# Kernel optimization log

Measured on AMD Instinct MI355X. Metric: run time of the kernel, lower is better.

Reference implementation:

```python
import jax, jax.numpy as jnp
import numpy as np

B, S, H, D = 32, 127, 4, 64
HD = H * D
SCALE = 1.0 / np.sqrt(D).astype(np.float32)
NEG = -100000.0


def _remove_mask_keep(seq_len):
    # For q>=3, rows are grouped in 2-row blocks starting at i=3,5,...;
    # each block may only attend (among k>=3) to its own two columns.
    q = jnp.arange(seq_len)[:, None]
    k = jnp.arange(seq_len)[None, :]
    blk = 3 + 2 * ((q - 3) // 2)
    return (q < 3) | (k < 3) | ((k >= blk) & (k < blk + 2))  # [S, S] bool


def setup_inputs() -> dict:
    rng = jax.random.key(0)
    ks = jax.random.split(rng, 16)
    n = lambda k, shape: jax.random.normal(k, shape, dtype=jnp.float32)
    w = 1.0 / np.sqrt(HD).astype(np.float32)
    return {
        "query": n(ks[0], (B, S, HD)),
        "key": n(ks[1], (B, S, HD)),
        "value": n(ks[2], (B, S, HD)),
        "graph": jax.random.randint(ks[3], (B, S, S), 0, 2, dtype=jnp.int32),
        "edge_key": n(ks[4], (B, S, S, D)),
        "edge_value": n(ks[5], (B, S, S, D)),
        "edge_query": n(ks[6], (B, S, S, D)),
        "Wq": n(ks[7], (HD, HD)) * w, "bq": jnp.zeros((HD,), jnp.float32),
        "Wk": n(ks[8], (HD, HD)) * w, "bk": jnp.zeros((HD,), jnp.float32),
        "Wv": n(ks[9], (HD, HD)) * w, "bv": jnp.zeros((HD,), jnp.float32),
        "Wo": n(ks[10], (HD, HD)) * w, "bo": jnp.zeros((HD,), jnp.float32),
    }


def reference(query, key, value, graph, edge_key, edge_value, edge_query,
              Wq, bq, Wk, bk, Wv, bv, Wo, bo):
    b, s, _ = query.shape
    q = (query @ Wq.T + bq).reshape(b, s, H, D)
    k = (key @ Wk.T + bk).reshape(b, s, H, D)
    v = (value @ Wv.T + bv).reshape(b, s, H, D)

    scores = (
        jnp.einsum('bqhd,bkhd->bhqk', q, k)
        + jnp.einsum('bqhd,bqkd->bhqk', q, edge_key)
        + jnp.einsum('bkqd,bkhd->bhqk', edge_query, k)
        + jnp.einsum('bkqd,bqkd->bqk', edge_query, edge_key)[:, None]
    ) * SCALE

    mask = (graph != 0)[:, None, :, :] & _remove_mask_keep(s)[None, None]
    scores = jnp.where(mask, scores, NEG)
    attn = jax.nn.softmax(scores, axis=-1)  # dropout p=0 -> identity

    x = (jnp.einsum('bhqk,bkhd->bqhd', attn, v)
         + jnp.einsum('bhqk,bqkd->bqhd', attn, edge_value)).reshape(b, s, HD)
    return x @ Wo.T + bo
```

## Files before the change

### kernel.cpp

```cpp
#include <hip/hip_runtime.h>
#include <hip/hip_bf16.h>

#define S_LEN 127
#define NB    32
#define HDIM  256
#define DH    64
#define SCALE_F 0.125f

typedef __bf16 bf16x8 __attribute__((ext_vector_type(8)));
typedef __bf16 bf16x4 __attribute__((ext_vector_type(4)));
typedef float  f32x4  __attribute__((ext_vector_type(4)));

#define NTOK  4064
#define NQKV4 260096
#define NW4   16384

__global__ __launch_bounds__(256) void convert_bf16(
    const float* __restrict__ q, const float* __restrict__ k,
    const float* __restrict__ v,
    const float* __restrict__ Wq, const float* __restrict__ Wk,
    const float* __restrict__ Wv, const float* __restrict__ Wo,
    __bf16* __restrict__ qb, __bf16* __restrict__ kb, __bf16* __restrict__ vb,
    __bf16* __restrict__ Wqb, __bf16* __restrict__ Wkb,
    __bf16* __restrict__ Wvb, __bf16* __restrict__ Wob)
{
  size_t t = (size_t)blockIdx.x * 256 + threadIdx.x;
  const float* src; __bf16* dst;
  if (t < NQKV4)               { src = q;  dst = qb;  }
  else if ((t -= NQKV4) < NQKV4) { src = k;  dst = kb;  }
  else if ((t -= NQKV4) < NQKV4) { src = v;  dst = vb;  }
  else if ((t -= NQKV4) < NW4)   { src = Wq; dst = Wqb; }
  else if ((t -= NW4) < NW4)     { src = Wk; dst = Wkb; }
  else if ((t -= NW4) < NW4)     { src = Wv; dst = Wvb; }
  else if ((t -= NW4) < NW4)     { src = Wo; dst = Wob; }
  else return;
  const float4 x = ((const float4*)src)[t];
  bf16x4 r;
  r[0] = (__bf16)x.x; r[1] = (__bf16)x.y; r[2] = (__bf16)x.z; r[3] = (__bf16)x.w;
  ((bf16x4*)dst)[t] = r;
}

__device__ __forceinline__ void gemm_tile32_bf16(
    const __bf16* __restrict__ A, const __bf16* __restrict__ W,
    const float* __restrict__ bias, float* __restrict__ out,
    int row0, int col0)
{
  const int lane = threadIdx.x & 63;
  const int r  = lane & 15;
  const int ks = (lane >> 4) << 3;
  const __bf16* Ab = A + (size_t)(row0 + r) * HDIM + ks;
  const __bf16* Wb = W + (size_t)(col0 + r) * HDIM + ks;
  f32x4 acc[2][2] = {};

  bf16x8 ca[2], cw[2];
  ca[0] = *(const bf16x8*)Ab;
  ca[1] = *(const bf16x8*)(Ab + (size_t)16 * HDIM);
  cw[0] = *(const bf16x8*)Wb;
  cw[1] = *(const bf16x8*)(Wb + (size_t)16 * HDIM);
#pragma unroll
  for (int kb = 0; kb < 8; ++kb) {
    bf16x8 na[2], nw[2];
    if (kb < 7) {
      const int off = (kb + 1) * 32;
      na[0] = *(const bf16x8*)(Ab + off);
      na[1] = *(const bf16x8*)(Ab + (size_t)16 * HDIM + off);
      nw[0] = *(const bf16x8*)(Wb + off);
      nw[1] = *(const bf16x8*)(Wb + (size_t)16 * HDIM + off);
    }
#pragma unroll
    for (int mi = 0; mi < 2; ++mi)
#pragma unroll
      for (int ni = 0; ni < 2; ++ni)
        acc[mi][ni] = __builtin_amdgcn_mfma_f32_16x16x32_bf16(
            ca[mi], cw[ni], acc[mi][ni], 0, 0, 0);
    if (kb < 7) {
      ca[0] = na[0]; ca[1] = na[1];
      cw[0] = nw[0]; cw[1] = nw[1];
    }
  }
  const int crow = (lane >> 4) * 4;
  const int ccol = lane & 15;
#pragma unroll
  for (int mi = 0; mi < 2; ++mi)
#pragma unroll
    for (int ni = 0; ni < 2; ++ni) {
      const int oc = col0 + ni * 16 + ccol;
      const float bv = bias[oc];
#pragma unroll
      for (int rg = 0; rg < 4; ++rg)
        out[(size_t)(row0 + mi * 16 + crow + rg) * HDIM + oc] = acc[mi][ni][rg] + bv;
    }
}

__global__ __launch_bounds__(256) void gemm_qkv(
    const __bf16* __restrict__ qb, const __bf16* __restrict__ kb,
    const __bf16* __restrict__ vb,
    const __bf16* __restrict__ Wqb, const float* __restrict__ bq,
    const __bf16* __restrict__ Wkb, const float* __restrict__ bk,
    const __bf16* __restrict__ Wvb, const float* __restrict__ bv,
    float* __restrict__ qp, float* __restrict__ kp, float* __restrict__ vp)
{
  const int w = threadIdx.x >> 6;
  const int tile = blockIdx.x * 4 + w;
  if (tile >= 127) return;
  const __bf16* A; const __bf16* W; const float* bias; float* o;
  if (blockIdx.z == 0)      { A = qb; W = Wqb; bias = bq; o = qp; }
  else if (blockIdx.z == 1) { A = kb; W = Wkb; bias = bk; o = kp; }
  else                      { A = vb; W = Wvb; bias = bv; o = vp; }
  gemm_tile32_bf16(A, W, bias, o, tile * 32, blockIdx.y * 32);
}

__global__ __launch_bounds__(256) void gemm_o(
    const __bf16* __restrict__ A, const __bf16* __restrict__ W,
    const float* __restrict__ bias, float* __restrict__ out)
{
  const int w = threadIdx.x >> 6;
  const int tile = blockIdx.x * 4 + w;
  if (tile >= 127) return;
  gemm_tile32_bf16(A, W, bias, out, tile * 32, blockIdx.y * 32);
}

__global__ __launch_bounds__(256) void attn_kernel(
    const float* __restrict__ qp, const float* __restrict__ kp,
    const float* __restrict__ vp, const int* __restrict__ graph,
    const float* __restrict__ ekt, const float* __restrict__ evt,
    const float* __restrict__ eqt, __bf16* __restrict__ xpb)
{
  int b, q;
  {
    const int bx = blockIdx.x;
    if (bx < 96) { b = bx / 3; q = bx % 3; }
    else { const int rr = bx - 96; b = rr / 124; q = 3 + rr % 124; }
  }
  const int t = threadIdx.x;
  const int w = t >> 6;
  const int l = t & 63;
  const int ll = l & 15;
  const int g  = l >> 4;

  __shared__ int   s_list[S_LEN];
  __shared__ float s_attn[4][S_LEN];
  __shared__ int   s_cnt[2];

  bool valid = false;
  const int k0 = w * 64 + l;
  if (w < 2 && k0 < S_LEN) {
    const int gr = graph[((size_t)b * S_LEN + q) * S_LEN + k0];
    bool keep;
    if (q < 3 || k0 < 3) keep = true;
    else {
      const int blk = 3 + 2 * ((q - 3) >> 1);
      keep = (k0 >= blk) & (k0 < blk + 2);
    }
    valid = (gr != 0) && keep;
  }
  const unsigned long long bal = __ballot(valid);
  if (w < 2 && l == 0) s_cnt[w] = (int)__popcll(bal);
  __syncthreads();
  int n = s_cnt[0] + s_cnt[1];
  if (valid) {
    const int pos = (int)__popcll(bal & ((1ull << l) - 1ull)) + (w ? s_cnt[0] : 0);
    s_list[pos] = k0;
  }
  __syncthreads();

  if (n == 0) {
    if (t < S_LEN) {
      s_list[t] = t;
      const float u = 1.0f / 127.0f;
      s_attn[0][t] = u; s_attn[1][t] = u; s_attn[2][t] = u; s_attn[3][t] = u;
    }
    n = S_LEN;
  } else {
    const float* qrow = qp + ((size_t)b * S_LEN + q) * HDIM;
    float4 q4[4];
#pragma unroll
    for (int h = 0; h < 4; ++h)
      q4[h] = *(const float4*)(qrow + h * 64 + ll * 4);
    const float* eqb = eqt + ((size_t)b * S_LEN * S_LEN + q) * DH;
    const float* ekb = ekt + ((size_t)(b * S_LEN + q)) * S_LEN * DH;
    const float* kpb = kp + (size_t)b * S_LEN * HDIM;

    for (int i0 = 0; i0 < n; i0 += 16) {
      const int i = i0 + w * 4 + g;
      float p0 = 0.f, p1 = 0.f, p2 = 0.f, p3 = 0.f;
      if (i < n) {
        const int kk = s_list[i];
        const float4 eq4 = *(const float4*)(eqb + (size_t)kk * (S_LEN * DH) + ll * 4);
        const float4 ek4 = *(const float4*)(ekb + kk * DH + ll * 4);
        const float* kr = kpb + (size_t)kk * HDIM + ll * 4;
        const float4 kh0 = *(const float4*)(kr);
        const float4 kh1 = *(const float4*)(kr + 64);
        const float4 kh2 = *(const float4*)(kr + 128);
        const float4 kh3 = *(const float4*)(kr + 192);
        const float tx = ek4.x, ty = ek4.y, tz = ek4.z, tw = ek4.w;
        const float s0x = q4[0].x + eq4.x, s0y = q4[0].y + eq4.y,
                    s0z = q4[0].z + eq4.z, s0w = q4[0].w + eq4.w;
        const float s1x = q4[1].x + eq4.x, s1y = q4[1].y + eq4.y,
                    s1z = q4[1].z + eq4.z, s1w = q4[1].w + eq4.w;
        const float s2x = q4[2].x + eq4.x, s2y = q4[2].y + eq4.y,
                    s2z = q4[2].z + eq4.z, s2w = q4[2].w + eq4.w;
        const float s3x = q4[3].x + eq4.x, s3y = q4[3].y + eq4.y,
                    s3z = q4[3].z + eq4.z, s3w = q4[3].w + eq4.w;
        p0 = s0x*(kh0.x+tx) + s0y*(kh0.y+ty) + s0z*(kh0.z+tz) + s0w*(kh0.w+tw);
        p1 = s1x*(kh1.x+tx) + s1y*(kh1.y+ty) + s1z*(kh1.z+tz) + s1w*(kh1.w+tw);
        p2 = s2x*(kh2.x+tx) + s2y*(kh2.y+ty) + s2z*(kh2.z+tz) + s2w*(kh2.w+tw);
        p3 = s3x*(kh3.x+tx) + s3y*(kh3.y+ty) + s3z*(kh3.z+tz) + s3w*(kh3.w+tw);
      }
#pragma unroll
      for (int off = 1; off < 16; off <<= 1) {
        p0 += __shfl_xor(p0, off, 64);
        p1 += __shfl_xor(p1, off, 64);
        p2 += __shfl_xor(p2, off, 64);
        p3 += __shfl_xor(p3, off, 64);
      }
      if (i < n && ll < 4) {
        const float s = (ll == 0) ? p0 : (ll == 1) ? p1 : (ll == 2) ? p2 : p3;
        s_attn[ll][i] = s * SCALE_F;
      }
    }
    __syncthreads();

    {
      const float v0 = (l < n) ? s_attn[w][l] : -INFINITY;
      const float v1 = (64 + l < n) ? s_attn[w][64 + l] : -INFINITY;
      float mx = fmaxf(v0, v1);
#pragma unroll
      for (int off = 32; off; off >>= 1) mx = fmaxf(mx, __shfl_xor(mx, off, 64));
      const float e0 = (l < n) ? expf(v0 - mx) : 0.f;
      const float e1 = (64 + l < n) ? expf(v1 - mx) : 0.f;
      float sm = e0 + e1;
#pragma unroll
      for (int off = 32; off; off >>= 1) sm += __shfl_xor(sm, off, 64);
      const float inv = 1.0f / sm;
      if (l < n) s_attn[w][l] = e0 * inv;
      if (64 + l < n) s_attn[w][64 + l] = e1 * inv;
    }
  }
  __syncthreads();

  {
    const float* evb = evt + ((size_t)(b * S_LEN + q)) * S_LEN * DH;
    const float* vbp = vp + (size_t)b * S_LEN * HDIM + w * DH + ll * 4;
    float ax = 0.f, ay = 0.f, az = 0.f, aw = 0.f;
    for (int i0 = 0; i0 < n; i0 += 4) {
      const int i = i0 + g;
      if (i < n) {
        const int kk = s_list[i];
        const float a = s_attn[w][i];
        const float4 v4 = *(const float4*)(vbp + (size_t)kk * HDIM);
        const float4 e4 = *(const float4*)(evb + kk * DH + ll * 4);
        ax += a * (v4.x + e4.x);
        ay += a * (v4.y + e4.y);
        az += a * (v4.z + e4.z);
        aw += a * (v4.w + e4.w);
      }
    }
#pragma unroll
    for (int off = 16; off < 64; off <<= 1) {
      ax += __shfl_xor(ax, off, 64);
      ay += __shfl_xor(ay, off, 64);
      az += __shfl_xor(az, off, 64);
      aw += __shfl_xor(aw, off, 64);
    }
    if (g == 0) {
      bf16x4 r;
      r[0] = (__bf16)ax; r[1] = (__bf16)ay; r[2] = (__bf16)az; r[3] = (__bf16)aw;
      *(bf16x4*)(xpb + ((size_t)b * S_LEN + q) * HDIM + w * 64 + ll * 4) = r;
    }
  }
}

extern "C" void kernel_launch(void* const* d_in, const int* in_sizes, int n_in,
                              void* d_out, int out_size, void* d_ws, size_t ws_size,
                              hipStream_t stream) {
  const float* query = (const float*)d_in[0];
  const float* key   = (const float*)d_in[1];
  const float* value = (const float*)d_in[2];
  const int*   graph = (const int*)d_in[3];
  const float* ekt   = (const float*)d_in[4];
  const float* evt   = (const float*)d_in[5];
  const float* eqt   = (const float*)d_in[6];
  const float* Wq = (const float*)d_in[7];  const float* bq = (const float*)d_in[8];
  const float* Wk = (const float*)d_in[9];  const float* bk = (const float*)d_in[10];
  const float* Wv = (const float*)d_in[11]; const float* bv = (const float*)d_in[12];
  const float* Wo = (const float*)d_in[13]; const float* bo = (const float*)d_in[14];
  float* out = (float*)d_out;

  const size_t NE = (size_t)NTOK * HDIM;
  char* p = (char*)d_ws;
  float* qp = (float*)p;            p += NE * 4;
  float* kp = (float*)p;            p += NE * 4;
  float* vp = (float*)p;            p += NE * 4;
  __bf16* qb  = (__bf16*)p;         p += NE * 2;
  __bf16* kb  = (__bf16*)p;         p += NE * 2;
  __bf16* vb  = (__bf16*)p;         p += NE * 2;
  __bf16* xpb = (__bf16*)p;         p += NE * 2;
  __bf16* Wqb = (__bf16*)p;         p += (size_t)HDIM * HDIM * 2;
  __bf16* Wkb = (__bf16*)p;         p += (size_t)HDIM * HDIM * 2;
  __bf16* Wvb = (__bf16*)p;         p += (size_t)HDIM * HDIM * 2;
  __bf16* Wob = (__bf16*)p;

  convert_bf16<<<dim3(3304), 256, 0, stream>>>(query, key, value,
                                               Wq, Wk, Wv, Wo,
                                               qb, kb, vb, Wqb, Wkb, Wvb, Wob);
  gemm_qkv<<<dim3(32, 8, 3), 256, 0, stream>>>(qb, kb, vb,
                                               Wqb, bq, Wkb, bk, Wvb, bv,
                                               qp, kp, vp);
  attn_kernel<<<dim3(NB * S_LEN), 256, 0, stream>>>(qp, kp, vp, graph,
                                                    ekt, evt, eqt, xpb);
  gemm_o<<<dim3(32, 8), 256, 0, stream>>>(xpb, Wob, bo, out);
}
```

Before: 52.76 us.

## Fuse activation bf16 conversion into QKV GEMM, store projections as bf16, prefetch attention loads

The QKV GEMM now reads the fp32 activations directly and converts them to bf16 into shared memory, so the separate activation-conversion pass and its bf16 copies are gone. Each block computes a 32x256 output tile with one wave per 64 columns. Q/K/V projections are stored as bf16 instead of fp32, which halves their write and gather traffic in the attention kernel. The attention score and value loops now software-prefetch the next iteration's gathered loads, at the cost of more registers and extra rounding of the projections.

```diff
diff --git a/kernel.cpp b/kernel.cpp
--- a/kernel.cpp
+++ b/kernel.cpp
@@ -12,39 +12,113 @@
 typedef float  f32x4  __attribute__((ext_vector_type(4)));
 
 #define NTOK  4064
-#define NQKV4 260096
 #define NW4   16384
 
-__global__ __launch_bounds__(256) void convert_bf16(
-    const float* __restrict__ q, const float* __restrict__ k,
-    const float* __restrict__ v,
+__device__ __forceinline__ float4 b2f4(bf16x4 v) {
+  return make_float4((float)v[0], (float)v[1], (float)v[2], (float)v[3]);
+}
+
+__global__ __launch_bounds__(256) void convert_w(
     const float* __restrict__ Wq, const float* __restrict__ Wk,
     const float* __restrict__ Wv, const float* __restrict__ Wo,
-    __bf16* __restrict__ qb, __bf16* __restrict__ kb, __bf16* __restrict__ vb,
     __bf16* __restrict__ Wqb, __bf16* __restrict__ Wkb,
     __bf16* __restrict__ Wvb, __bf16* __restrict__ Wob)
 {
   size_t t = (size_t)blockIdx.x * 256 + threadIdx.x;
   const float* src; __bf16* dst;
-  if (t < NQKV4)               { src = q;  dst = qb;  }
-  else if ((t -= NQKV4) < NQKV4) { src = k;  dst = kb;  }
-  else if ((t -= NQKV4) < NQKV4) { src = v;  dst = vb;  }
-  else if ((t -= NQKV4) < NW4)   { src = Wq; dst = Wqb; }
-  else if ((t -= NW4) < NW4)     { src = Wk; dst = Wkb; }
-  else if ((t -= NW4) < NW4)     { src = Wv; dst = Wvb; }
-  else if ((t -= NW4) < NW4)     { src = Wo; dst = Wob; }
-  else return;
+  if (t < NW4)                 { src = Wq; dst = Wqb; }
+  else if ((t -= NW4) < NW4)   { src = Wk; dst = Wkb; }
+  else if ((t -= NW4) < NW4)   { src = Wv; dst = Wvb; }
+  else { t -= NW4;               src = Wo; dst = Wob; }
   const float4 x = ((const float4*)src)[t];
   bf16x4 r;
   r[0] = (__bf16)x.x; r[1] = (__bf16)x.y; r[2] = (__bf16)x.z; r[3] = (__bf16)x.w;
   ((bf16x4*)dst)[t] = r;
 }
 
-__device__ __forceinline__ void gemm_tile32_bf16(
+__global__ __launch_bounds__(256) void gemm_qkv(
+    const float* __restrict__ q_in, const float* __restrict__ k_in,
+    const float* __restrict__ v_in,
+    const __bf16* __restrict__ Wqb, const float* __restrict__ bq,
+    const __bf16* __restrict__ Wkb, const float* __restrict__ bk,
+    const __bf16* __restrict__ Wvb, const float* __restrict__ bv,
+    __bf16* __restrict__ qpb, __bf16* __restrict__ kpb, __bf16* __restrict__ vpb)
+{
+  const int tile = blockIdx.x;
+  const float* A; const __bf16* W; const float* bias; __bf16* o;
+  if (blockIdx.y == 0)      { A = q_in; W = Wqb; bias = bq; o = qpb; }
+  else if (blockIdx.y == 1) { A = k_in; W = Wkb; bias = bk; o = kpb; }
+  else                      { A = v_in; W = Wvb; bias = bv; o = vpb; }
+
+  __shared__ __bf16 sA[32][264];
+  const int row0 = tile * 32;
+
+#pragma unroll
+  for (int j = 0; j < 8; ++j) {
+    const int f = threadIdx.x + j * 256;
+    const int rr = f >> 6, c4 = f & 63;
+    const float4 x = *(const float4*)(A + (size_t)(row0 + rr) * HDIM + c4 * 4);
+    __bf16* d = &sA[rr][c4 * 4];
+    d[0] = (__bf16)x.x; d[1] = (__bf16)x.y; d[2] = (__bf16)x.z; d[3] = (__bf16)x.w;
+  }
+  __syncthreads();
+
+  const int w    = threadIdx.x >> 6;
+  const int lane = threadIdx.x & 63;
+  const int r    = lane & 15;
+  const int ksl  = (lane >> 4) << 3;
+  const int wc   = w * 64;
+
+  const __bf16* Wb = W + (size_t)(wc + r) * HDIM + ksl;
+  f32x4 acc[2][4] = {};
+
+  bf16x8 cw[4];
+#pragma unroll
+  for (int ni = 0; ni < 4; ++ni)
+    cw[ni] = *(const bf16x8*)(Wb + (size_t)ni * 16 * HDIM);
+#pragma unroll
+  for (int kb = 0; kb < 8; ++kb) {
+    bf16x8 nw[4];
+    if (kb < 7) {
+#pragma unroll
+      for (int ni = 0; ni < 4; ++ni)
+        nw[ni] = *(const bf16x8*)(Wb + (size_t)ni * 16 * HDIM + (kb + 1) * 32);
+    }
+    const bf16x8 a0 = *(const bf16x8*)&sA[r][kb * 32 + ksl];
+    const bf16x8 a1 = *(const bf16x8*)&sA[16 + r][kb * 32 + ksl];
+#pragma unroll
+    for (int ni = 0; ni < 4; ++ni) {
+      acc[0][ni] = __builtin_amdgcn_mfma_f32_16x16x32_bf16(a0, cw[ni], acc[0][ni], 0, 0, 0);
+      acc[1][ni] = __builtin_amdgcn_mfma_f32_16x16x32_bf16(a1, cw[ni], acc[1][ni], 0, 0, 0);
+    }
+    if (kb < 7) {
+#pragma unroll
+      for (int ni = 0; ni < 4; ++ni) cw[ni] = nw[ni];
+    }
+  }
+  const int crow = (lane >> 4) * 4;
+  const int ccol = lane & 15;
+#pragma unroll
+  for (int mi = 0; mi < 2; ++mi)
+#pragma unroll
+    for (int ni = 0; ni < 4; ++ni) {
+      const int oc = wc + ni * 16 + ccol;
+      const float bv = bias[oc];
+#pragma unroll
+      for (int rg = 0; rg < 4; ++rg)
+        o[(size_t)(row0 + mi * 16 + crow + rg) * HDIM + oc] =
+            (__bf16)(acc[mi][ni][rg] + bv);
+    }
+}
+
+__global__ __launch_bounds__(256) void gemm_o(
     const __bf16* __restrict__ A, const __bf16* __restrict__ W,
-    const float* __restrict__ bias, float* __restrict__ out,
-    int row0, int col0)
+    const float* __restrict__ bias, float* __restrict__ out)
 {
+  const int w = threadIdx.x >> 6;
+  const int tile = blockIdx.x * 4 + w;
+  if (tile >= 127) return;
+  const int row0 = tile * 32, col0 = blockIdx.y * 32;
   const int lane = threadIdx.x & 63;
   const int r  = lane & 15;
   const int ks = (lane >> 4) << 3;
@@ -92,37 +166,9 @@
     }
 }
 
-__global__ __launch_bounds__(256) void gemm_qkv(
-    const __bf16* __restrict__ qb, const __bf16* __restrict__ kb,
-    const __bf16* __restrict__ vb,
-    const __bf16* __restrict__ Wqb, const float* __restrict__ bq,
-    const __bf16* __restrict__ Wkb, const float* __restrict__ bk,
-    const __bf16* __restrict__ Wvb, const float* __restrict__ bv,
-    float* __restrict__ qp, float* __restrict__ kp, float* __restrict__ vp)
-{
-  const int w = threadIdx.x >> 6;
-  const int tile = blockIdx.x * 4 + w;
-  if (tile >= 127) return;
-  const __bf16* A; const __bf16* W; const float* bias; float* o;
-  if (blockIdx.z == 0)      { A = qb; W = Wqb; bias = bq; o = qp; }
-  else if (blockIdx.z == 1) { A = kb; W = Wkb; bias = bk; o = kp; }
-  else                      { A = vb; W = Wvb; bias = bv; o = vp; }
-  gemm_tile32_bf16(A, W, bias, o, tile * 32, blockIdx.y * 32);
-}
-
-__global__ __launch_bounds__(256) void gemm_o(
-    const __bf16* __restrict__ A, const __bf16* __restrict__ W,
-    const float* __restrict__ bias, float* __restrict__ out)
-{
-  const int w = threadIdx.x >> 6;
-  const int tile = blockIdx.x * 4 + w;
-  if (tile >= 127) return;
-  gemm_tile32_bf16(A, W, bias, out, tile * 32, blockIdx.y * 32);
-}
-
 __global__ __launch_bounds__(256) void attn_kernel(
-    const float* __restrict__ qp, const float* __restrict__ kp,
-    const float* __restrict__ vp, const int* __restrict__ graph,
+    const __bf16* __restrict__ qpb, const __bf16* __restrict__ kpb,
+    const __bf16* __restrict__ vpb, const int* __restrict__ graph,
     const float* __restrict__ ekt, const float* __restrict__ evt,
     const float* __restrict__ eqt, __bf16* __restrict__ xpb)
 {
@@ -172,40 +218,55 @@
     }
     n = S_LEN;
   } else {
-    const float* qrow = qp + ((size_t)b * S_LEN + q) * HDIM;
+    const __bf16* qrow = qpb + ((size_t)b * S_LEN + q) * HDIM;
     float4 q4[4];
 #pragma unroll
     for (int h = 0; h < 4; ++h)
-      q4[h] = *(const float4*)(qrow + h * 64 + ll * 4);
-    const float* eqb = eqt + ((size_t)b * S_LEN * S_LEN + q) * DH;
-    const float* ekb = ekt + ((size_t)(b * S_LEN + q)) * S_LEN * DH;
-    const float* kpb = kp + (size_t)b * S_LEN * HDIM;
-
+      q4[h] = b2f4(*(const bf16x4*)(qrow + h * 64 + ll * 4));
+    const float* eqb2 = eqt + ((size_t)b * S_LEN * S_LEN + q) * DH;
+    const float* ekb2 = ekt + ((size_t)(b * S_LEN + q)) * S_LEN * DH;
+    const __bf16* kpbb = kpb + (size_t)b * S_LEN * HDIM;
+    const int myi = w * 4 + g;
+
+    float4 ceq, cek;
+    bf16x4 ck0, ck1, ck2, ck3;
+    if (myi < n) {
+      const int kk = s_list[myi];
+      ceq = *(const float4*)(eqb2 + (size_t)kk * (S_LEN * DH) + ll * 4);
+      cek = *(const float4*)(ekb2 + kk * DH + ll * 4);
+      const __bf16* kr = kpbb + (size_t)kk * HDIM + ll * 4;
+      ck0 = *(const bf16x4*)(kr);
+      ck1 = *(const bf16x4*)(kr + 64);
+      ck2 = *(const bf16x4*)(kr + 128);
+      ck3 = *(const bf16x4*)(kr + 192);
+    }
     for (int i0 = 0; i0 < n; i0 += 16) {
-      const int i = i0 + w * 4 + g;
+      const int i = i0 + myi;
+      float4 neq, nek;
+      bf16x4 nk0, nk1, nk2, nk3;
+      const int j = i + 16;
+      if (j < n) {
+        const int kk = s_list[j];
+        neq = *(const float4*)(eqb2 + (size_t)kk * (S_LEN * DH) + ll * 4);
+        nek = *(const float4*)(ekb2 + kk * DH + ll * 4);
+        const __bf16* kr = kpbb + (size_t)kk * HDIM + ll * 4;
+        nk0 = *(const bf16x4*)(kr);
+        nk1 = *(const bf16x4*)(kr + 64);
+        nk2 = *(const bf16x4*)(kr + 128);
+        nk3 = *(const bf16x4*)(kr + 192);
+      }
       float p0 = 0.f, p1 = 0.f, p2 = 0.f, p3 = 0.f;
       if (i < n) {
-        const int kk = s_list[i];
-        const float4 eq4 = *(const float4*)(eqb + (size_t)kk * (S_LEN * DH) + ll * 4);
-        const float4 ek4 = *(const float4*)(ekb + kk * DH + ll * 4);
-        const float* kr = kpb + (size_t)kk * HDIM + ll * 4;
-        const float4 kh0 = *(const float4*)(kr);
-        const float4 kh1 = *(const float4*)(kr + 64);
-        const float4 kh2 = *(const float4*)(kr + 128);
-        const float4 kh3 = *(const float4*)(kr + 192);
-        const float tx = ek4.x, ty = ek4.y, tz = ek4.z, tw = ek4.w;
-        const float s0x = q4[0].x + eq4.x, s0y = q4[0].y + eq4.y,
-                    s0z = q4[0].z + eq4.z, s0w = q4[0].w + eq4.w;
-        const float s1x = q4[1].x + eq4.x, s1y = q4[1].y + eq4.y,
-                    s1z = q4[1].z + eq4.z, s1w = q4[1].w + eq4.w;
-        const float s2x = q4[2].x + eq4.x, s2y = q4[2].y + eq4.y,
-                    s2z = q4[2].z + eq4.z, s2w = q4[2].w + eq4.w;
-        const float s3x = q4[3].x + eq4.x, s3y = q4[3].y + eq4.y,
-                    s3z = q4[3].z + eq4.z, s3w = q4[3].w + eq4.w;
-        p0 = s0x*(kh0.x+tx) + s0y*(kh0.y+ty) + s0z*(kh0.z+tz) + s0w*(kh0.w+tw);
-        p1 = s1x*(kh1.x+tx) + s1y*(kh1.y+ty) + s1z*(kh1.z+tz) + s1w*(kh1.w+tw);
-        p2 = s2x*(kh2.x+tx) + s2y*(kh2.y+ty) + s2z*(kh2.z+tz) + s2w*(kh2.w+tw);
-        p3 = s3x*(kh3.x+tx) + s3y*(kh3.y+ty) + s3z*(kh3.z+tz) + s3w*(kh3.w+tw);
+        const float4 k0f = b2f4(ck0), k1f = b2f4(ck1),
+                     k2f = b2f4(ck2), k3f = b2f4(ck3);
+        p0 = (q4[0].x+ceq.x)*(k0f.x+cek.x) + (q4[0].y+ceq.y)*(k0f.y+cek.y)
+           + (q4[0].z+ceq.z)*(k0f.z+cek.z) + (q4[0].w+ceq.w)*(k0f.w+cek.w);
+        p1 = (q4[1].x+ceq.x)*(k1f.x+cek.x) + (q4[1].y+ceq.y)*(k1f.y+cek.y)
+           + (q4[1].z+ceq.z)*(k1f.z+cek.z) + (q4[1].w+ceq.w)*(k1f.w+cek.w);
+        p2 = (q4[2].x+ceq.x)*(k2f.x+cek.x) + (q4[2].y+ceq.y)*(k2f.y+cek.y)
+           + (q4[2].z+ceq.z)*(k2f.z+cek.z) + (q4[2].w+ceq.w)*(k2f.w+cek.w);
+        p3 = (q4[3].x+ceq.x)*(k3f.x+cek.x) + (q4[3].y+ceq.y)*(k3f.y+cek.y)
+           + (q4[3].z+ceq.z)*(k3f.z+cek.z) + (q4[3].w+ceq.w)*(k3f.w+cek.w);
       }
 #pragma unroll
       for (int off = 1; off < 16; off <<= 1) {
@@ -218,6 +279,8 @@
         const float s = (ll == 0) ? p0 : (ll == 1) ? p1 : (ll == 2) ? p2 : p3;
         s_attn[ll][i] = s * SCALE_F;
       }
+      ceq = neq; cek = nek;
+      ck0 = nk0; ck1 = nk1; ck2 = nk2; ck3 = nk3;
     }
     __syncthreads();
 
@@ -240,33 +303,46 @@
   __syncthreads();
 
   {
-    const float* evb = evt + ((size_t)(b * S_LEN + q)) * S_LEN * DH;
-    const float* vbp = vp + (size_t)b * S_LEN * HDIM + w * DH + ll * 4;
-    float ax = 0.f, ay = 0.f, az = 0.f, aw = 0.f;
-    for (int i0 = 0; i0 < n; i0 += 4) {
-      const int i = i0 + g;
-      if (i < n) {
-        const int kk = s_list[i];
-        const float a = s_attn[w][i];
-        const float4 v4 = *(const float4*)(vbp + (size_t)kk * HDIM);
-        const float4 e4 = *(const float4*)(evb + kk * DH + ll * 4);
-        ax += a * (v4.x + e4.x);
-        ay += a * (v4.y + e4.y);
-        az += a * (v4.z + e4.z);
-        aw += a * (v4.w + e4.w);
-      }
+    const float* evb2 = evt + ((size_t)(b * S_LEN + q)) * S_LEN * DH;
+    const __bf16* vbp = vpb + (size_t)b * S_LEN * HDIM + w * DH + ll * 4;
+    float ax = 0.f, ay = 0.f, az = 0.f, aw2 = 0.f;
+
+    int i = g;
+    float a = 0.f; bf16x4 v4; float4 e4;
+    if (i < n) {
+      const int kk = s_list[i];
+      a = s_attn[w][i];
+      v4 = *(const bf16x4*)(vbp + (size_t)kk * HDIM);
+      e4 = *(const float4*)(evb2 + kk * DH + ll * 4);
+    }
+    while (i < n) {
+      const int j = i + 4;
+      float a2 = 0.f; bf16x4 v42; float4 e42;
+      if (j < n) {
+        const int kk = s_list[j];
+        a2 = s_attn[w][j];
+        v42 = *(const bf16x4*)(vbp + (size_t)kk * HDIM);
+        e42 = *(const float4*)(evb2 + kk * DH + ll * 4);
+      }
+      const float4 vf = b2f4(v4);
+      ax  += a * (vf.x + e4.x);
+      ay  += a * (vf.y + e4.y);
+      az  += a * (vf.z + e4.z);
+      aw2 += a * (vf.w + e4.w);
+      i = j; a = a2; v4 = v42; e4 = e42;
     }
 #pragma unroll
     for (int off = 16; off < 64; off <<= 1) {
-      ax += __shfl_xor(ax, off, 64);
-      ay += __shfl_xor(ay, off, 64);
-      az += __shfl_xor(az, off, 64);
-      aw += __shfl_xor(aw, off, 64);
+      ax  += __shfl_xor(ax, off, 64);
+      ay  += __shfl_xor(ay, off, 64);
+      az  += __shfl_xor(az, off, 64);
+      aw2 += __shfl_xor(aw2, off, 64);
     }
     if (g == 0) {
-      bf16x4 r;
-      r[0] = (__bf16)ax; r[1] = (__bf16)ay; r[2] = (__bf16)az; r[3] = (__bf16)aw;
-      *(bf16x4*)(xpb + ((size_t)b * S_LEN + q) * HDIM + w * 64 + ll * 4) = r;
+      bf16x4 rr;
+      rr[0] = (__bf16)ax; rr[1] = (__bf16)ay;
+      rr[2] = (__bf16)az; rr[3] = (__bf16)aw2;
+      *(bf16x4*)(xpb + ((size_t)b * S_LEN + q) * HDIM + w * 64 + ll * 4) = rr;
     }
   }
 }
@@ -289,25 +365,20 @@
 
   const size_t NE = (size_t)NTOK * HDIM;
   char* p = (char*)d_ws;
-  float* qp = (float*)p;            p += NE * 4;
-  float* kp = (float*)p;            p += NE * 4;
-  float* vp = (float*)p;            p += NE * 4;
-  __bf16* qb  = (__bf16*)p;         p += NE * 2;
-  __bf16* kb  = (__bf16*)p;         p += NE * 2;
-  __bf16* vb  = (__bf16*)p;         p += NE * 2;
+  __bf16* qpb = (__bf16*)p;         p += NE * 2;
+  __bf16* kpb = (__bf16*)p;         p += NE * 2;
+  __bf16* vpb = (__bf16*)p;         p += NE * 2;
   __bf16* xpb = (__bf16*)p;         p += NE * 2;
   __bf16* Wqb = (__bf16*)p;         p += (size_t)HDIM * HDIM * 2;
   __bf16* Wkb = (__bf16*)p;         p += (size_t)HDIM * HDIM * 2;
   __bf16* Wvb = (__bf16*)p;         p += (size_t)HDIM * HDIM * 2;
   __bf16* Wob = (__bf16*)p;
 
-  convert_bf16<<<dim3(3304), 256, 0, stream>>>(query, key, value,
-                                               Wq, Wk, Wv, Wo,
-                                               qb, kb, vb, Wqb, Wkb, Wvb, Wob);
-  gemm_qkv<<<dim3(32, 8, 3), 256, 0, stream>>>(qb, kb, vb,
-                                               Wqb, bq, Wkb, bk, Wvb, bv,
-                                               qp, kp, vp);
-  attn_kernel<<<dim3(NB * S_LEN), 256, 0, stream>>>(qp, kp, vp, graph,
+  convert_w<<<dim3(256), 256, 0, stream>>>(Wq, Wk, Wv, Wo, Wqb, Wkb, Wvb, Wob);
+  gemm_qkv<<<dim3(127, 3), 256, 0, stream>>>(query, key, value,
+                                             Wqb, bq, Wkb, bk, Wvb, bv,
+                                             qpb, kpb, vpb);
+  attn_kernel<<<dim3(NB * S_LEN), 256, 0, stream>>>(qpb, kpb, vpb, graph,
                                                     ekt, evt, eqt, xpb);
   gemm_o<<<dim3(32, 8), 256, 0, stream>>>(xpb, Wob, bo, out);
 }
```

Result: no change. 51.99 us (-1.5%).
